# Performance work log

Measured on AMD Instinct MI355X. Metric: run time of the kernel, lower is better.

Reference implementation:

```python
import jax, jax.numpy as jnp
import numpy as np

NUM_HEADS = 16
ROPE_BASE = 10000.0


def apply_rope(x):
    # x: [B, T, H, D]; torchtune-style interleaved-pair RoPE, positions 0..T-1
    B, T, H, D = x.shape
    inv_freq = 1.0 / (ROPE_BASE ** (jnp.arange(0, D, 2, dtype=jnp.float32) / D))  # [D/2]
    pos = jnp.arange(T, dtype=jnp.float32)
    freqs = pos[:, None] * inv_freq[None, :]              # [T, D/2]
    cos = jnp.cos(freqs)[None, :, None, :].astype(x.dtype)
    sin = jnp.sin(freqs)[None, :, None, :].astype(x.dtype)
    x1 = x[..., 0::2]
    x2 = x[..., 1::2]
    o1 = x1 * cos - x2 * sin
    o2 = x2 * cos + x1 * sin
    return jnp.stack([o1, o2], axis=-1).reshape(B, T, H, D)


def setup_inputs() -> dict:
    key = jax.random.key(0)
    k1, k2, k3 = jax.random.split(key, 3)
    B, T, C = 2, 8192, 1024
    x = jax.random.normal(k1, (B, T, C), dtype=jnp.float32)
    # torch Linear weight layout [out_features, in_features]; fan-in scaling
    Wqkv = jax.random.normal(k2, (3 * C, C), dtype=jnp.float32) * (C ** -0.5)
    Wout = jax.random.normal(k3, (C, C), dtype=jnp.float32) * (C ** -0.5)
    return {"x": x, "Wqkv": Wqkv, "Wout": Wout}


def reference(x, Wqkv, Wout):
    B, T, C = x.shape
    H = NUM_HEADS
    D = C // H
    qkv = (x @ Wqkv.T).reshape(B, T, 3, H, D)
    q, k, v = qkv[:, :, 0], qkv[:, :, 1], qkv[:, :, 2]   # each [B, T, H, D]
    q = apply_rope(q)
    k = apply_rope(k)
    # Faithful to source: SDPA is called on [B, T, H, D] WITHOUT transposing,
    # so torch attends over the heads axis (L = H) with (B, T) as batch dims.
    scale = 1.0 / jnp.sqrt(jnp.asarray(D, dtype=x.dtype))
    scores = jnp.einsum('btqd,btkd->btqk', q, k) * scale  # [B, T, H, H]
    attn = jax.nn.softmax(scores, axis=-1)
    out = jnp.einsum('btqk,btkd->btqd', attn, v)          # [B, T, H, D]
    # Replicate attn_output.transpose(1, 2).contiguous().view(B, T, C)
    out = out.transpose(0, 2, 1, 3).reshape(B, T, C)
    return out @ Wout.T
```

## Files before the change

### kernel.cpp

```cpp
#include <hip/hip_runtime.h>
#include <stdint.h>

#define TT 8192
#define BT 16384
#define MCH 8192

typedef __attribute__((ext_vector_type(8))) __bf16 bf16x8;
typedef __attribute__((ext_vector_type(4))) __bf16 bf16x4;
typedef __attribute__((ext_vector_type(4))) short short4v;
typedef __attribute__((ext_vector_type(4))) float floatx4;

__device__ __forceinline__ float bf2f(unsigned short h) {
  union { unsigned u; float f; } x; x.u = ((unsigned)h) << 16; return x.f;
}
__device__ __forceinline__ unsigned short f2bf(float f) {
  union { float f; unsigned u; } x; x.f = f;
  unsigned r = (x.u + 0x7fffu + ((x.u >> 16) & 1u)) >> 16;
  return (unsigned short)r;
}
__device__ __forceinline__ void async16(const void* g, void* l) {
  __builtin_amdgcn_global_load_lds(
      (__attribute__((address_space(1))) void*)g,
      (__attribute__((address_space(3))) void*)l, 16, 0, 0);
}

__global__ __launch_bounds__(256) void cvt_f2b(
    const float* __restrict__ src, unsigned short* __restrict__ dst, int n4) {
  const int i = blockIdx.x * 256 + threadIdx.x;
  if (i < n4) {
    const float4 f = ((const float4*)src)[i];
    union { uint2 u2; unsigned short s[4]; } o;
    o.s[0] = f2bf(f.x); o.s[1] = f2bf(f.y);
    o.s[2] = f2bf(f.z); o.s[3] = f2bf(f.w);
    ((uint2*)dst)[i] = o.u2;
  }
}

__global__ __launch_bounds__(256) void rope_table_k(float2* __restrict__ tab) {
  const int i = blockIdx.x * 256 + threadIdx.x;
  if (i < TT * 32) {
    const int t = i >> 5, p = i & 31;
    const float f = (float)t * exp2f((float)p * -0.41524101186092f);
    float s, c;
    sincosf(f, &s, &c);
    tab[i] = make_float2(c, s);
  }
}

template <bool CF32>
__global__ __launch_bounds__(256) void gemm_bt(
    const unsigned short* __restrict__ A,
    const unsigned short* __restrict__ W,
    void* __restrict__ C,
    int M, int N, int K)
{
  __shared__ __align__(16) unsigned short As[128 * 32];
  __shared__ __align__(16) unsigned short Bs[128 * 32];

  const int tid  = threadIdx.x;
  const int lane = tid & 63;
  const int w    = tid >> 6;
  const int nb   = N / 128;
  const int bm   = blockIdx.x / nb;
  const int bn   = blockIdx.x % nb;
  const int wm   = w & 1;
  const int wn   = w >> 1;
  const int kg   = lane >> 4;
  const int lm   = lane & 15;
  const int srow = lane >> 2;
  const int sch  = lane & 3;

  floatx4 acc[4][4];
  floatx4 z = {0.f, 0.f, 0.f, 0.f};
#pragma unroll
  for (int i = 0; i < 4; ++i)
#pragma unroll
    for (int j = 0; j < 4; ++j) acc[i][j] = z;

  const size_t abase = (size_t)(bm * 128) * K;
  const size_t bbase = (size_t)(bn * 128) * K;

  for (int kt = 0; kt < K; kt += 32) {
#pragma unroll
    for (int s2 = 0; s2 < 2; ++s2) {
      const int s   = 2 * w + s2;
      const int row = 16 * s + srow;
      async16(A + abase + (size_t)row * K + kt + sch * 8, (char*)As + s * 1024);
      async16(W + bbase + (size_t)row * K + kt + sch * 8, (char*)Bs + s * 1024);
    }
    __syncthreads();

    bf16x8 af[4], bfr[4];
#pragma unroll
    for (int i = 0; i < 4; ++i) {
      const int r = wm * 64 + i * 16 + lm;
      af[i] = *(const bf16x8*)(As + r * 32 + kg * 8);
    }
#pragma unroll
    for (int j = 0; j < 4; ++j) {
      const int r = wn * 64 + j * 16 + lm;
      bfr[j] = *(const bf16x8*)(Bs + r * 32 + kg * 8);
    }
#pragma unroll
    for (int i = 0; i < 4; ++i)
#pragma unroll
      for (int j = 0; j < 4; ++j)
        acc[i][j] = __builtin_amdgcn_mfma_f32_16x16x32_bf16(af[i], bfr[j], acc[i][j], 0, 0, 0);
    __syncthreads();
  }

#pragma unroll
  for (int i = 0; i < 4; ++i) {
    const int row0 = bm * 128 + wm * 64 + i * 16 + kg * 4;
#pragma unroll
    for (int j = 0; j < 4; ++j) {
      const int col = bn * 128 + wn * 64 + j * 16 + lm;
#pragma unroll
      for (int r = 0; r < 4; ++r) {
        if (CF32)
          ((float*)C)[(size_t)(row0 + r) * N + col] = acc[i][j][r];
        else
          ((unsigned short*)C)[(size_t)(row0 + r) * N + col] = f2bf(acc[i][j][r]);
      }
    }
  }
}

#if defined(__has_builtin)
#if __has_builtin(__builtin_amdgcn_mfma_f32_16x16x16_bf16)
#define PV_MFMA 1
#define PV_MFMA_CALL(a, b, c) __builtin_amdgcn_mfma_f32_16x16x16_bf16( \
    *(bf16x4*)&(a), *(bf16x4*)&(b), (c), 0, 0, 0)
#elif __has_builtin(__builtin_amdgcn_mfma_f32_16x16x16bf16_1k)
#define PV_MFMA 1
#define PV_MFMA_CALL(a, b, c) __builtin_amdgcn_mfma_f32_16x16x16bf16_1k( \
    (a), (b), (c), 0, 0, 0)
#else
#define PV_MFMA 0
#endif
#else
#define PV_MFMA 0
#endif

__global__ __launch_bounds__(128) void attn_rope_k(
    const unsigned short* __restrict__ qkv,
    const float2* __restrict__ tab,
    unsigned short* __restrict__ Y,
    int base)
{
  __shared__ __align__(16) unsigned short sQKV[2][3 * 16 * 72];
#if !PV_MFMA
  __shared__ float sP[2][256];
#endif

  const int wave = threadIdx.x >> 6;
  const int lane = threadIdx.x & 63;
  const int ml = blockIdx.x * 2 + wave;
  const int m  = base + ml;
  const int t  = m & (TT - 1);
  const int b  = m >> 13;

  unsigned short* QB = sQKV[wave];
  unsigned short* KB = QB + 16 * 72;
  unsigned short* VB = QB + 2 * 16 * 72;

  const int lm   = lane & 15;
  const int quad = lane >> 4;

  const uint4* row = (const uint4*)(qkv + (size_t)ml * 3072);
#pragma unroll
  for (int i = 0; i < 6; ++i) {
    const int c = lane + 64 * i;
    union { uint4 u4; unsigned short s[8]; } cv;
    cv.u4 = row[c];
    const int n0   = c * 8;
    const int part = n0 >> 10;
    const int h    = (n0 >> 6) & 15;
    const int d0   = n0 & 63;
    if (part < 2) {
      float f[8];
#pragma unroll
      for (int j = 0; j < 8; ++j) f[j] = bf2f(cv.s[j]);
      const int p0 = d0 >> 1;
      const float4 csA = *(const float4*)(tab + (t << 5) + p0);
      const float4 csB = *(const float4*)(tab + (t << 5) + p0 + 2);
      const float cs[4] = {csA.x, csA.z, csB.x, csB.z};
      const float sn[4] = {csA.y, csA.w, csB.y, csB.w};
#pragma unroll
      for (int j = 0; j < 4; ++j) {
        const float x1 = f[2 * j], x2 = f[2 * j + 1];
        cv.s[2 * j]     = f2bf(x1 * cs[j] - x2 * sn[j]);
        cv.s[2 * j + 1] = f2bf(x2 * cs[j] + x1 * sn[j]);
      }
    }
    unsigned short* dst = QB + part * (16 * 72) + h * 72 + d0;
    *(uint4*)dst = cv.u4;
  }
  __syncthreads();

  floatx4 accS = {0.f, 0.f, 0.f, 0.f};
#pragma unroll
  for (int half = 0; half < 2; ++half) {
    const bf16x8 kf = *(const bf16x8*)(KB + lm * 72 + half * 32 + quad * 8);
    const bf16x8 qf = *(const bf16x8*)(QB + lm * 72 + half * 32 + quad * 8);
    accS = __builtin_amdgcn_mfma_f32_16x16x32_bf16(kf, qf, accS, 0, 0, 0);
  }
  float s4[4];
  float mx = -1e30f;
#pragma unroll
  for (int j = 0; j < 4; ++j) { s4[j] = accS[j] * 0.125f; mx = fmaxf(mx, s4[j]); }
  mx = fmaxf(mx, __shfl_xor(mx, 16, 64));
  mx = fmaxf(mx, __shfl_xor(mx, 32, 64));
  float sum = 0.f;
#pragma unroll
  for (int j = 0; j < 4; ++j) { s4[j] = __expf(s4[j] - mx); sum += s4[j]; }
  sum += __shfl_xor(sum, 16, 64);
  sum += __shfl_xor(sum, 32, 64);
  const float inv = 1.0f / sum;

#if PV_MFMA
  union { short4v v; unsigned short s[4]; } pf;
#pragma unroll
  for (int j = 0; j < 4; ++j) pf.s[j] = s4[j] * inv == 0.f ? 0 : f2bf(s4[j] * inv);
#pragma unroll
  for (int dtile = 0; dtile < 4; ++dtile) {
    union { short4v v; unsigned short s[4]; } vf;
#pragma unroll
    for (int j = 0; j < 4; ++j)
      vf.s[j] = VB[(quad * 4 + j) * 72 + dtile * 16 + lm];
    floatx4 accO = {0.f, 0.f, 0.f, 0.f};
    accO = PV_MFMA_CALL(pf.v, vf.v, accO);
    const int col = (t & 15) * 64 + dtile * 16 + lm;
#pragma unroll
    for (int r = 0; r < 4; ++r) {
      const size_t rr = (size_t)b * TT + (size_t)(quad * 4 + r) * 512 + (t >> 4);
      Y[rr * 1024 + col] = f2bf(accO[r]);
    }
  }
#else
  float* P = sP[wave];
#pragma unroll
  for (int j = 0; j < 4; ++j) P[(quad * 4 + j) * 16 + lm] = s4[j] * inv;
  __syncthreads();
  float o[16];
#pragma unroll
  for (int dd = 0; dd < 16; ++dd) o[dd] = 0.f;
#pragma unroll
  for (int kh = 0; kh < 16; ++kh) {
    const float a = P[kh * 16 + lm];
    union { uint4 u4; unsigned short s[8]; } v0, v1;
    v0.u4 = *(const uint4*)(VB + kh * 72 + quad * 16);
    v1.u4 = *(const uint4*)(VB + kh * 72 + quad * 16 + 8);
#pragma unroll
    for (int dd = 0; dd < 8; ++dd) {
      o[dd]     += a * bf2f(v0.s[dd]);
      o[dd + 8] += a * bf2f(v1.s[dd]);
    }
  }
  const size_t rr = (size_t)b * TT + (size_t)lm * 512 + (t >> 4);
  unsigned short* yp = Y + rr * 1024 + (t & 15) * 64 + quad * 16;
  union { uint4 u4; unsigned short s[8]; } o1, o2;
#pragma unroll
  for (int dd = 0; dd < 8; ++dd) o1.s[dd] = f2bf(o[dd]);
#pragma unroll
  for (int dd = 0; dd < 8; ++dd) o2.s[dd] = f2bf(o[8 + dd]);
  ((uint4*)yp)[0] = o1.u4;
  ((uint4*)yp)[1] = o2.u4;
#endif
}

extern "C" void kernel_launch(void* const* d_in, const int* in_sizes, int n_in,
                              void* d_out, int out_size, void* d_ws, size_t ws_size,
                              hipStream_t stream) {
  const float* x    = (const float*)d_in[0];
  const float* Wqkv = (const float*)d_in[1];
  const float* Wout = (const float*)d_in[2];
  float* out = (float*)d_out;

  unsigned short* Y     = (unsigned short*)d_ws;
  unsigned short* Wqkvb = Y + (size_t)BT * 1024;
  unsigned short* Woutb = Wqkvb + (size_t)3072 * 1024;
  unsigned short* xb    = Woutb + (size_t)1024 * 1024;
  unsigned short* qkvC  = (unsigned short*)d_out;
  float2* tab           = (float2*)((char*)d_out + (size_t)52 * 1024 * 1024);

  rope_table_k<<<dim3(TT * 32 / 256), dim3(256), 0, stream>>>(tab);
  cvt_f2b<<<dim3(3072 * 1024 / 4 / 256), dim3(256), 0, stream>>>(Wqkv, Wqkvb, 3072 * 1024 / 4);
  cvt_f2b<<<dim3(1024 * 1024 / 4 / 256), dim3(256), 0, stream>>>(Wout, Woutb, 1024 * 1024 / 4);

  for (int base = 0; base < BT; base += MCH) {
    cvt_f2b<<<dim3(MCH * 1024 / 4 / 256), dim3(256), 0, stream>>>(
        x + (size_t)base * 1024, xb, MCH * 1024 / 4);
    gemm_bt<false><<<dim3((MCH / 128) * (3072 / 128)), dim3(256), 0, stream>>>(
        xb, Wqkvb, qkvC, MCH, 3072, 1024);
    attn_rope_k<<<dim3(MCH / 2), dim3(128), 0, stream>>>(qkvC, tab, Y, base);
  }

  gemm_bt<true><<<dim3((BT / 128) * (1024 / 128)), dim3(256), 0, stream>>>(
      Y, Woutb, out, BT, 1024, 1024);
}
```

Baseline: 357.3 us.

## Replace GEMM with 256x256-tile double-buffered pipelined kernel with swizzled LDS

Replaces the 128x128, single-buffered, K=32 GEMM with a 256x256 tile kernel using 8 waves and a K-step of 64. It double-buffers LDS with staggered async global-to-LDS loads, XOR-swizzles LDS columns to avoid bank conflicts, and remaps block IDs for cache locality. It also raises MFMA priority and uses fine-grained waitcnt and barriers so loads overlap compute. The aim is to raise MFMA utilisation and cut the load-then-sync stalls of the old kernel, at the cost of more LDS and registers per block and fewer, larger blocks.

```diff
diff --git a/kernel.cpp b/kernel.cpp
--- a/kernel.cpp
+++ b/kernel.cpp
@@ -48,73 +48,136 @@
 }
 
 template <bool CF32>
-__global__ __launch_bounds__(256) void gemm_bt(
+__global__ __launch_bounds__(512, 2) void gemm256(
     const unsigned short* __restrict__ A,
     const unsigned short* __restrict__ W,
     void* __restrict__ C,
     int M, int N, int K)
 {
-  __shared__ __align__(16) unsigned short As[128 * 32];
-  __shared__ __align__(16) unsigned short Bs[128 * 32];
+  __shared__ __align__(16) unsigned short sm[2][2][256 * 64];
 
   const int tid  = threadIdx.x;
   const int lane = tid & 63;
-  const int w    = tid >> 6;
-  const int nb   = N / 128;
-  const int bm   = blockIdx.x / nb;
-  const int bn   = blockIdx.x % nb;
-  const int wm   = w & 1;
-  const int wn   = w >> 1;
+  const int wid  = tid >> 6;
+  const int wr   = wid >> 2;
+  const int wc   = wid & 3;
+  const int lm   = lane & 15;
   const int kg   = lane >> 4;
-  const int lm   = lane & 15;
-  const int srow = lane >> 2;
-  const int sch  = lane & 3;
-
-  floatx4 acc[4][4];
+
+  const int nb  = N >> 8;
+  const int cpx = (int)gridDim.x >> 3;
+  const int bid = blockIdx.x;
+  const int swz = (bid & 7) * cpx + (bid >> 3);
+  const int bm  = swz / nb;
+  const int bn  = swz % nb;
+
+  const int NT = K >> 6;
+
+  const int srow = lane >> 3;
+  const int sc   = (lane & 7) ^ srow;
+
+  auto stage = [&](const unsigned short* __restrict__ G, size_t grow0,
+                   int kcol, unsigned short* lds) {
+#pragma unroll
+    for (int q = 0; q < 2; ++q) {
+      const int seg = q * 8 + wid;
+      const int r   = seg * 8 + srow;
+      async16(G + (grow0 + (size_t)r) * (size_t)K + kcol + sc * 8,
+              (char*)lds + seg * 1024);
+    }
+  };
+
+  floatx4 acc[8][4];
   floatx4 z = {0.f, 0.f, 0.f, 0.f};
 #pragma unroll
-  for (int i = 0; i < 4; ++i)
+  for (int i = 0; i < 8; ++i)
 #pragma unroll
     for (int j = 0; j < 4; ++j) acc[i][j] = z;
 
-  const size_t abase = (size_t)(bm * 128) * K;
-  const size_t bbase = (size_t)(bn * 128) * K;
-
-  for (int kt = 0; kt < K; kt += 32) {
-#pragma unroll
-    for (int s2 = 0; s2 < 2; ++s2) {
-      const int s   = 2 * w + s2;
-      const int row = 16 * s + srow;
-      async16(A + abase + (size_t)row * K + kt + sch * 8, (char*)As + s * 1024);
-      async16(W + bbase + (size_t)row * K + kt + sch * 8, (char*)Bs + s * 1024);
-    }
-    __syncthreads();
-
-    bf16x8 af[4], bfr[4];
-#pragma unroll
-    for (int i = 0; i < 4; ++i) {
-      const int r = wm * 64 + i * 16 + lm;
-      af[i] = *(const bf16x8*)(As + r * 32 + kg * 8);
-    }
+  const size_t arow = (size_t)bm * 256;
+  const size_t brow = (size_t)bn * 256;
+
+  stage(A, arow,       0, &sm[0][0][0]);
+  stage(A, arow + 128, 0, &sm[0][0][128 * 64]);
+  stage(W, brow,       0, &sm[0][1][0]);
+  stage(W, brow + 128, 0, &sm[0][1][128 * 64]);
+  if (NT > 1) {
+    stage(W, brow,       64, &sm[1][1][0]);
+    stage(W, brow + 128, 64, &sm[1][1][128 * 64]);
+  }
+  asm volatile("s_waitcnt vmcnt(4)" ::: "memory");
+  __builtin_amdgcn_s_barrier();
+  __builtin_amdgcn_sched_barrier(0);
+
+  const int cxor = lm & 7;
+
+  for (int t = 0; t < NT; ++t) {
+    const int buf = t & 1;
+    const unsigned short* Ab = &sm[buf][0][0];
+    const unsigned short* Bb = &sm[buf][1][0];
+    bf16x8 bfrag[4][2];
+
+#pragma unroll
+    for (int p = 0; p < 4; ++p) {
+      bf16x8 afrag[2][2];
+#pragma unroll
+      for (int ii = 0; ii < 2; ++ii) {
+        const int rr = wr * 128 + (p * 2 + ii) * 16 + lm;
+#pragma unroll
+        for (int kk = 0; kk < 2; ++kk)
+          afrag[ii][kk] =
+              *(const bf16x8*)(Ab + rr * 64 + (((kk << 2) + kg) ^ cxor) * 8);
+      }
+      if (p == 0) {
+#pragma unroll
+        for (int j = 0; j < 4; ++j) {
+          const int rr = wc * 64 + j * 16 + lm;
+#pragma unroll
+          for (int kk = 0; kk < 2; ++kk)
+            bfrag[j][kk] =
+                *(const bf16x8*)(Bb + rr * 64 + (((kk << 2) + kg) ^ cxor) * 8);
+        }
+      }
+
+      if (p < 2) {
+        if (t + 1 < NT)
+          stage(A, arow + p * 128, (t + 1) * 64,
+                &sm[buf ^ 1][0][p * 128 * 64]);
+      } else {
+        if (t + 2 < NT)
+          stage(W, brow + (p - 2) * 128, (t + 2) * 64,
+                &sm[buf][1][(p - 2) * 128 * 64]);
+      }
+
+      __builtin_amdgcn_s_barrier();
+      asm volatile("s_waitcnt lgkmcnt(0)" ::: "memory");
+      __builtin_amdgcn_sched_barrier(0);
+
+      __builtin_amdgcn_s_setprio(1);
+#pragma unroll
+      for (int ii = 0; ii < 2; ++ii)
+#pragma unroll
+        for (int j = 0; j < 4; ++j)
+#pragma unroll
+          for (int kk = 0; kk < 2; ++kk)
+            acc[p * 2 + ii][j] = __builtin_amdgcn_mfma_f32_16x16x32_bf16(
+                afrag[ii][kk], bfrag[j][kk], acc[p * 2 + ii][j], 0, 0, 0);
+      __builtin_amdgcn_s_setprio(0);
+
+      if (p == 3) {
+        asm volatile("s_waitcnt vmcnt(4)" ::: "memory");
+      }
+      __builtin_amdgcn_s_barrier();
+      if (p == 3) __builtin_amdgcn_sched_barrier(0);
+    }
+  }
+
+#pragma unroll
+  for (int i = 0; i < 8; ++i) {
+    const int row0 = bm * 256 + wr * 128 + i * 16 + kg * 4;
 #pragma unroll
     for (int j = 0; j < 4; ++j) {
-      const int r = wn * 64 + j * 16 + lm;
-      bfr[j] = *(const bf16x8*)(Bs + r * 32 + kg * 8);
-    }
-#pragma unroll
-    for (int i = 0; i < 4; ++i)
-#pragma unroll
-      for (int j = 0; j < 4; ++j)
-        acc[i][j] = __builtin_amdgcn_mfma_f32_16x16x32_bf16(af[i], bfr[j], acc[i][j], 0, 0, 0);
-    __syncthreads();
-  }
-
-#pragma unroll
-  for (int i = 0; i < 4; ++i) {
-    const int row0 = bm * 128 + wm * 64 + i * 16 + kg * 4;
-#pragma unroll
-    for (int j = 0; j < 4; ++j) {
-      const int col = bn * 128 + wn * 64 + j * 16 + lm;
+      const int col = bn * 256 + wc * 64 + j * 16 + lm;
 #pragma unroll
       for (int r = 0; r < 4; ++r) {
         if (CF32)
@@ -291,11 +354,11 @@
   for (int base = 0; base < BT; base += MCH) {
     cvt_f2b<<<dim3(MCH * 1024 / 4 / 256), dim3(256), 0, stream>>>(
         x + (size_t)base * 1024, xb, MCH * 1024 / 4);
-    gemm_bt<false><<<dim3((MCH / 128) * (3072 / 128)), dim3(256), 0, stream>>>(
+    gemm256<false><<<dim3((MCH / 256) * (3072 / 256)), dim3(512), 0, stream>>>(
         xb, Wqkvb, qkvC, MCH, 3072, 1024);
     attn_rope_k<<<dim3(MCH / 2), dim3(128), 0, stream>>>(qkvC, tab, Y, base);
   }
 
-  gemm_bt<true><<<dim3((BT / 128) * (1024 / 128)), dim3(256), 0, stream>>>(
+  gemm256<true><<<dim3((BT / 256) * (1024 / 256)), dim3(512), 0, stream>>>(
       Y, Woutb, out, BT, 1024, 1024);
 }
```

Measured after the change: 321.9 us. -9.9%, faster.

## Double-buffer GEMM LDS tiles with 256x128 blocks, XOR swizzle, block remap

Applied to the files above, without the earlier changes.

Replaces the single-buffered 128x128 GEMM with a 512-thread, 256x128-tile kernel. The kernel double-buffers LDS and prefetches two K-tiles ahead with async global-to-LDS loads, using explicit waitcnt and barriers instead of two full syncthreads per iteration. It also XOR-swizzles LDS columns to cut bank conflicts, remaps block IDs across 8 groups for cache locality, and raises wave priority around the MFMA block. The goal is to hide global load latency behind compute, at the cost of more LDS per block and hand-managed synchronisation that is fragile to get right.

```diff
diff --git a/kernel.cpp b/kernel.cpp
--- a/kernel.cpp
+++ b/kernel.cpp
@@ -48,27 +48,56 @@
 }
 
 template <bool CF32>
-__global__ __launch_bounds__(256) void gemm_bt(
+__global__ __launch_bounds__(512, 4) void gemm_k32(
     const unsigned short* __restrict__ A,
     const unsigned short* __restrict__ W,
     void* __restrict__ C,
     int M, int N, int K)
 {
-  __shared__ __align__(16) unsigned short As[128 * 32];
-  __shared__ __align__(16) unsigned short Bs[128 * 32];
+  __shared__ __align__(16) unsigned short sm[2][(256 + 128) * 32];
 
   const int tid  = threadIdx.x;
   const int lane = tid & 63;
-  const int w    = tid >> 6;
-  const int nb   = N / 128;
-  const int bm   = blockIdx.x / nb;
-  const int bn   = blockIdx.x % nb;
-  const int wm   = w & 1;
-  const int wn   = w >> 1;
+  const int wid  = tid >> 6;
+  const int wr   = wid >> 1;
+  const int wc   = wid & 1;
+  const int lm   = lane & 15;
   const int kg   = lane >> 4;
-  const int lm   = lane & 15;
-  const int srow = lane >> 2;
-  const int sch  = lane & 3;
+  const int cxor = (lm >> 1) & 3;
+
+  const int nb  = N >> 7;
+  const int cpx = (int)gridDim.x >> 3;
+  const int bid = blockIdx.x;
+  const int swz = (bid & 7) * cpx + (bid >> 3);
+  const int bm  = swz / nb;
+  const int bn  = swz % nb;
+
+  const int NT = K >> 5;
+
+  const int sr  = lane >> 2;
+  const int scb = lane & 3;
+  const unsigned short* gsrc0;
+  const unsigned short* gsrc1;
+  const unsigned short* gsrc2;
+  {
+    const int r0 = wid * 16 + sr;
+    const int r1 = 128 + r0;
+    const int rB = wid * 16 + sr;
+    gsrc0 = A + (size_t)(bm * 256 + r0) * (size_t)K + ((scb ^ ((r0 >> 1) & 3)) << 3);
+    gsrc1 = A + (size_t)(bm * 256 + r1) * (size_t)K + ((scb ^ ((r1 >> 1) & 3)) << 3);
+    gsrc2 = W + (size_t)(bn * 128 + rB) * (size_t)K + ((scb ^ ((rB >> 1) & 3)) << 3);
+  }
+  const int ld0 = wid * 1024;
+  const int ld1 = 8192 + wid * 1024;
+  const int ld2 = 16384 + wid * 1024;
+
+  auto stage_tile = [&](int tt) {
+    char* lb = (char*)sm[tt & 1];
+    const size_t koff = (size_t)tt << 5;
+    async16(gsrc0 + koff, lb + ld0);
+    async16(gsrc1 + koff, lb + ld1);
+    async16(gsrc2 + koff, lb + ld2);
+  };
 
   floatx4 acc[4][4];
   floatx4 z = {0.f, 0.f, 0.f, 0.f};
@@ -77,44 +106,59 @@
 #pragma unroll
     for (int j = 0; j < 4; ++j) acc[i][j] = z;
 
-  const size_t abase = (size_t)(bm * 128) * K;
-  const size_t bbase = (size_t)(bn * 128) * K;
-
-  for (int kt = 0; kt < K; kt += 32) {
-#pragma unroll
-    for (int s2 = 0; s2 < 2; ++s2) {
-      const int s   = 2 * w + s2;
-      const int row = 16 * s + srow;
-      async16(A + abase + (size_t)row * K + kt + sch * 8, (char*)As + s * 1024);
-      async16(W + bbase + (size_t)row * K + kt + sch * 8, (char*)Bs + s * 1024);
-    }
-    __syncthreads();
+  stage_tile(0);
+  stage_tile(1);
+  asm volatile("s_waitcnt vmcnt(3)" ::: "memory");
+  __builtin_amdgcn_s_barrier();
+  __builtin_amdgcn_sched_barrier(0);
+
+  for (int t = 0; t < NT; ++t) {
+    const unsigned short* Ab = sm[t & 1];
+    const unsigned short* Bb = Ab + 256 * 32;
 
     bf16x8 af[4], bfr[4];
 #pragma unroll
     for (int i = 0; i < 4; ++i) {
-      const int r = wm * 64 + i * 16 + lm;
-      af[i] = *(const bf16x8*)(As + r * 32 + kg * 8);
+      const int rr = wr * 64 + i * 16 + lm;
+      af[i] = *(const bf16x8*)(Ab + rr * 32 + ((kg ^ cxor) << 3));
     }
 #pragma unroll
     for (int j = 0; j < 4; ++j) {
-      const int r = wn * 64 + j * 16 + lm;
-      bfr[j] = *(const bf16x8*)(Bs + r * 32 + kg * 8);
-    }
+      const int rr = wc * 64 + j * 16 + lm;
+      bfr[j] = *(const bf16x8*)(Bb + rr * 32 + ((kg ^ cxor) << 3));
+    }
+
+    __builtin_amdgcn_s_barrier();
+    asm volatile("s_waitcnt lgkmcnt(0)" ::: "memory");
+    __builtin_amdgcn_sched_barrier(0);
+
+    if (t + 2 < NT) stage_tile(t + 2);
+
+    __builtin_amdgcn_s_setprio(1);
 #pragma unroll
     for (int i = 0; i < 4; ++i)
 #pragma unroll
       for (int j = 0; j < 4; ++j)
-        acc[i][j] = __builtin_amdgcn_mfma_f32_16x16x32_bf16(af[i], bfr[j], acc[i][j], 0, 0, 0);
-    __syncthreads();
+        acc[i][j] = __builtin_amdgcn_mfma_f32_16x16x32_bf16(
+            af[i], bfr[j], acc[i][j], 0, 0, 0);
+    __builtin_amdgcn_s_setprio(0);
+
+    if (t + 1 < NT) {
+      if (t + 2 < NT)
+        asm volatile("s_waitcnt vmcnt(3)" ::: "memory");
+      else
+        asm volatile("s_waitcnt vmcnt(0)" ::: "memory");
+      __builtin_amdgcn_s_barrier();
+      __builtin_amdgcn_sched_barrier(0);
+    }
   }
 
 #pragma unroll
   for (int i = 0; i < 4; ++i) {
-    const int row0 = bm * 128 + wm * 64 + i * 16 + kg * 4;
+    const int row0 = bm * 256 + wr * 64 + i * 16 + kg * 4;
 #pragma unroll
     for (int j = 0; j < 4; ++j) {
-      const int col = bn * 128 + wn * 64 + j * 16 + lm;
+      const int col = bn * 128 + wc * 64 + j * 16 + lm;
 #pragma unroll
       for (int r = 0; r < 4; ++r) {
         if (CF32)
@@ -291,11 +335,11 @@
   for (int base = 0; base < BT; base += MCH) {
     cvt_f2b<<<dim3(MCH * 1024 / 4 / 256), dim3(256), 0, stream>>>(
         x + (size_t)base * 1024, xb, MCH * 1024 / 4);
-    gemm_bt<false><<<dim3((MCH / 128) * (3072 / 128)), dim3(256), 0, stream>>>(
+    gemm_k32<false><<<dim3((MCH / 256) * (3072 / 128)), dim3(512), 0, stream>>>(
         xb, Wqkvb, qkvC, MCH, 3072, 1024);
     attn_rope_k<<<dim3(MCH / 2), dim3(128), 0, stream>>>(qkvC, tab, Y, base);
   }
 
-  gemm_bt<true><<<dim3((BT / 128) * (1024 / 128)), dim3(256), 0, stream>>>(
+  gemm_k32<true><<<dim3((BT / 256) * (1024 / 128)), dim3(512), 0, stream>>>(
       Y, Woutb, out, BT, 1024, 1024);
 }
```

Result: faster. 311.7 us (-12.8%).

## Rewrite GEMMs with pre-packed weight fragments, triple-buffered swizzled A tiles, larger blocks

Applied to the files above, without the earlier changes.

Weights are now packed once into an MFMA-fragment-ordered bf16 layout, so each wave loads its B fragments directly from global memory into registers, double-buffered, and no longer stages them through LDS. A tiles of 256 rows are staged asynchronously into a three-deep LDS ring with an XOR swizzle to avoid bank conflicts. Explicit vmcnt waits and a single barrier per k-step give a software pipeline. Blocks grow to 512 threads with 256x192 or 256x128 tiles, a grid swizzle improves L2 locality, and setprio is raised around the MFMA bursts. This cuts LDS traffic and barrier stalls, at the cost of higher register pressure and fragile hand-tuned waitcnt counts.

```diff
diff --git a/kernel.cpp b/kernel.cpp
--- a/kernel.cpp
+++ b/kernel.cpp
@@ -36,6 +36,25 @@
   }
 }
 
+__global__ __launch_bounds__(256) void pack_w(
+    const float* __restrict__ src, uint4* __restrict__ dst, int nchunks,
+    int K, int NT) {
+  const int c = blockIdx.x * 256 + threadIdx.x;
+  if (c >= nchunks) return;
+  const int l  = c & 63;
+  const int g  = c >> 6;
+  const int kt = g % NT;
+  const int rb = g / NT;
+  const int row = rb * 16 + (l & 15);
+  const int k0  = kt * 32 + (l >> 4) * 8;
+  const float4 f0 = *(const float4*)(src + (size_t)row * K + k0);
+  const float4 f1 = *(const float4*)(src + (size_t)row * K + k0 + 4);
+  union { uint4 u4; unsigned short s[8]; } o;
+  o.s[0] = f2bf(f0.x); o.s[1] = f2bf(f0.y); o.s[2] = f2bf(f0.z); o.s[3] = f2bf(f0.w);
+  o.s[4] = f2bf(f1.x); o.s[5] = f2bf(f1.y); o.s[6] = f2bf(f1.z); o.s[7] = f2bf(f1.w);
+  dst[c] = o.u4;
+}
+
 __global__ __launch_bounds__(256) void rope_table_k(float2* __restrict__ tab) {
   const int i = blockIdx.x * 256 + threadIdx.x;
   if (i < TT * 32) {
@@ -47,74 +66,132 @@
   }
 }
 
-template <bool CF32>
-__global__ __launch_bounds__(256) void gemm_bt(
+template <int NWF, bool CF32>
+__global__ __launch_bounds__(512, 2) void gemm_bd(
     const unsigned short* __restrict__ A,
-    const unsigned short* __restrict__ W,
+    const uint4* __restrict__ Wp,
     void* __restrict__ C,
     int M, int N, int K)
 {
-  __shared__ __align__(16) unsigned short As[128 * 32];
-  __shared__ __align__(16) unsigned short Bs[128 * 32];
-
+  __shared__ __align__(16) unsigned short smA[3 * 256 * 32];
+
+  const int BN   = 2 * NWF * 16;
   const int tid  = threadIdx.x;
   const int lane = tid & 63;
-  const int w    = tid >> 6;
-  const int nb   = N / 128;
-  const int bm   = blockIdx.x / nb;
-  const int bn   = blockIdx.x % nb;
-  const int wm   = w & 1;
-  const int wn   = w >> 1;
+  const int wid  = tid >> 6;
+  const int wr   = wid >> 1;
+  const int wcl  = wid & 1;
+  const int lm   = lane & 15;
   const int kg   = lane >> 4;
-  const int lm   = lane & 15;
-  const int srow = lane >> 2;
-  const int sch  = lane & 3;
-
-  floatx4 acc[4][4];
+  const int cxor = (lm >> 1) & 3;
+
+  const int nbm = M >> 8;
+  const int cpx = (int)gridDim.x >> 3;
+  const int bid = blockIdx.x;
+  const int swz = (bid & 7) * cpx + (bid >> 3);
+  const int bm  = swz % nbm;
+  const int bn  = swz / nbm;
+
+  const int NT = K >> 5;
+
+  const unsigned short* gsrcA0;
+  const unsigned short* gsrcA1;
+  int ldso0, ldso1;
+  {
+    const int i0 = tid, i1 = 512 + tid;
+    const int r0 = i0 >> 2, c0 = i0 & 3;
+    const int r1 = i1 >> 2, c1 = i1 & 3;
+    gsrcA0 = A + (size_t)(bm * 256 + r0) * (size_t)K + ((c0 ^ ((r0 >> 1) & 3)) << 3);
+    gsrcA1 = A + (size_t)(bm * 256 + r1) * (size_t)K + ((c1 ^ ((r1 >> 1) & 3)) << 3);
+    ldso0 = i0 * 8;
+    ldso1 = i1 * 8;
+  }
+#define STAGE_A(tt)                                                      \
+  {                                                                      \
+    unsigned short* d = smA + ((tt) % 3) * 8192;                         \
+    async16(gsrcA0 + (size_t)(tt) * 32, d + ldso0);                      \
+    async16(gsrcA1 + (size_t)(tt) * 32, d + ldso1);                      \
+  }
+
+  const int rbg0 = bn * (BN >> 4) + wcl * NWF;
+  const uint4* WpJ[NWF];
+#pragma unroll
+  for (int j = 0; j < NWF; ++j)
+    WpJ[j] = Wp + ((size_t)(rbg0 + j) * (size_t)NT) * 64 + lane;
+
+  floatx4 acc[4][NWF];
   floatx4 z = {0.f, 0.f, 0.f, 0.f};
 #pragma unroll
   for (int i = 0; i < 4; ++i)
 #pragma unroll
-    for (int j = 0; j < 4; ++j) acc[i][j] = z;
-
-  const size_t abase = (size_t)(bm * 128) * K;
-  const size_t bbase = (size_t)(bn * 128) * K;
-
-  for (int kt = 0; kt < K; kt += 32) {
-#pragma unroll
-    for (int s2 = 0; s2 < 2; ++s2) {
-      const int s   = 2 * w + s2;
-      const int row = 16 * s + srow;
-      async16(A + abase + (size_t)row * K + kt + sch * 8, (char*)As + s * 1024);
-      async16(W + bbase + (size_t)row * K + kt + sch * 8, (char*)Bs + s * 1024);
-    }
-    __syncthreads();
-
-    bf16x8 af[4], bfr[4];
-#pragma unroll
-    for (int i = 0; i < 4; ++i) {
-      const int r = wm * 64 + i * 16 + lm;
-      af[i] = *(const bf16x8*)(As + r * 32 + kg * 8);
-    }
-#pragma unroll
-    for (int j = 0; j < 4; ++j) {
-      const int r = wn * 64 + j * 16 + lm;
-      bfr[j] = *(const bf16x8*)(Bs + r * 32 + kg * 8);
-    }
-#pragma unroll
-    for (int i = 0; i < 4; ++i)
-#pragma unroll
-      for (int j = 0; j < 4; ++j)
-        acc[i][j] = __builtin_amdgcn_mfma_f32_16x16x32_bf16(af[i], bfr[j], acc[i][j], 0, 0, 0);
-    __syncthreads();
-  }
+    for (int j = 0; j < NWF; ++j) acc[i][j] = z;
+
+  bf16x8 Bbuf0[NWF], Bbuf1[NWF];
+
+#pragma unroll
+  for (int j = 0; j < NWF; ++j)
+    Bbuf0[j] = *(const bf16x8*)(WpJ[j]);
+  STAGE_A(0);
+  STAGE_A(1);
+  asm volatile("s_waitcnt vmcnt(2)" ::: "memory");
+  __builtin_amdgcn_sched_barrier(0);
+
+#define SUBITER(T, BC, BNX)                                                   \
+  {                                                                           \
+    const int t_ = (T);                                                       \
+    __builtin_amdgcn_s_barrier();                                             \
+    const unsigned short* Ab = smA + (t_ % 3) * 8192;                         \
+    bf16x8 afr[4];                                                            \
+    _Pragma("unroll")                                                         \
+    for (int i = 0; i < 4; ++i) {                                             \
+      const int rr = wr * 64 + i * 16 + lm;                                   \
+      afr[i] = *(const bf16x8*)(Ab + rr * 32 + ((kg ^ cxor) << 3));           \
+    }                                                                         \
+    if (t_ + 1 < NT) {                                                        \
+      _Pragma("unroll")                                                       \
+      for (int j = 0; j < NWF; ++j)                                           \
+        BNX[j] = *(const bf16x8*)(WpJ[j] + (size_t)(t_ + 1) * 64);            \
+    }                                                                         \
+    if (t_ + 2 < NT) STAGE_A(t_ + 2);                                         \
+    if (t_ + 2 < NT) {                                                        \
+      if constexpr (NWF == 6)                                                 \
+        asm volatile("s_waitcnt vmcnt(8)" ::: "memory");                      \
+      else                                                                    \
+        asm volatile("s_waitcnt vmcnt(6)" ::: "memory");                      \
+    } else if (t_ + 1 < NT) {                                                 \
+      if constexpr (NWF == 6)                                                 \
+        asm volatile("s_waitcnt vmcnt(6)" ::: "memory");                      \
+      else                                                                    \
+        asm volatile("s_waitcnt vmcnt(4)" ::: "memory");                      \
+    } else {                                                                  \
+      asm volatile("s_waitcnt vmcnt(0)" ::: "memory");                        \
+    }                                                                         \
+    asm volatile("s_waitcnt lgkmcnt(0)" ::: "memory");                        \
+    __builtin_amdgcn_sched_barrier(0);                                        \
+    __builtin_amdgcn_s_setprio(1);                                            \
+    _Pragma("unroll")                                                         \
+    for (int i = 0; i < 4; ++i)                                               \
+      _Pragma("unroll")                                                       \
+      for (int j = 0; j < NWF; ++j)                                           \
+        acc[i][j] = __builtin_amdgcn_mfma_f32_16x16x32_bf16(                  \
+            afr[i], BC[j], acc[i][j], 0, 0, 0);                               \
+    __builtin_amdgcn_s_setprio(0);                                            \
+    __builtin_amdgcn_sched_barrier(0);                                        \
+  }
+
+  for (int t = 0; t < NT; t += 2) {
+    SUBITER(t, Bbuf0, Bbuf1);
+    SUBITER(t + 1, Bbuf1, Bbuf0);
+  }
+#undef SUBITER
+#undef STAGE_A
 
 #pragma unroll
   for (int i = 0; i < 4; ++i) {
-    const int row0 = bm * 128 + wm * 64 + i * 16 + kg * 4;
-#pragma unroll
-    for (int j = 0; j < 4; ++j) {
-      const int col = bn * 128 + wn * 64 + j * 16 + lm;
+    const int row0 = bm * 256 + wr * 64 + i * 16 + kg * 4;
+#pragma unroll
+    for (int j = 0; j < NWF; ++j) {
+      const int col = bn * BN + wcl * (NWF * 16) + j * 16 + lm;
 #pragma unroll
       for (int r = 0; r < 4; ++r) {
         if (CF32)
@@ -278,24 +355,26 @@
   float* out = (float*)d_out;
 
   unsigned short* Y     = (unsigned short*)d_ws;
-  unsigned short* Wqkvb = Y + (size_t)BT * 1024;
-  unsigned short* Woutb = Wqkvb + (size_t)3072 * 1024;
-  unsigned short* xb    = Woutb + (size_t)1024 * 1024;
+  unsigned short* Wqkvp = Y + (size_t)BT * 1024;
+  unsigned short* Woutp = Wqkvp + (size_t)3072 * 1024;
+  unsigned short* xb    = Woutp + (size_t)1024 * 1024;
   unsigned short* qkvC  = (unsigned short*)d_out;
   float2* tab           = (float2*)((char*)d_out + (size_t)52 * 1024 * 1024);
 
   rope_table_k<<<dim3(TT * 32 / 256), dim3(256), 0, stream>>>(tab);
-  cvt_f2b<<<dim3(3072 * 1024 / 4 / 256), dim3(256), 0, stream>>>(Wqkv, Wqkvb, 3072 * 1024 / 4);
-  cvt_f2b<<<dim3(1024 * 1024 / 4 / 256), dim3(256), 0, stream>>>(Wout, Woutb, 1024 * 1024 / 4);
+  pack_w<<<dim3(3072 * 1024 / 8 / 256), dim3(256), 0, stream>>>(
+      Wqkv, (uint4*)Wqkvp, 3072 * 1024 / 8, 1024, 32);
+  pack_w<<<dim3(1024 * 1024 / 8 / 256), dim3(256), 0, stream>>>(
+      Wout, (uint4*)Woutp, 1024 * 1024 / 8, 1024, 32);
 
   for (int base = 0; base < BT; base += MCH) {
     cvt_f2b<<<dim3(MCH * 1024 / 4 / 256), dim3(256), 0, stream>>>(
         x + (size_t)base * 1024, xb, MCH * 1024 / 4);
-    gemm_bt<false><<<dim3((MCH / 128) * (3072 / 128)), dim3(256), 0, stream>>>(
-        xb, Wqkvb, qkvC, MCH, 3072, 1024);
+    gemm_bd<6, false><<<dim3((MCH / 256) * (3072 / 192)), dim3(512), 0, stream>>>(
+        xb, (const uint4*)Wqkvp, qkvC, MCH, 3072, 1024);
     attn_rope_k<<<dim3(MCH / 2), dim3(128), 0, stream>>>(qkvC, tab, Y, base);
   }
 
-  gemm_bt<true><<<dim3((BT / 128) * (1024 / 128)), dim3(256), 0, stream>>>(
-      Y, Woutb, out, BT, 1024, 1024);
-}
+  gemm_bd<4, true><<<dim3((BT / 256) * (1024 / 128)), dim3(512), 0, stream>>>(
+      Y, (const uint4*)Woutp, out, BT, 1024, 1024);
+}
```

Result: slower. 365.9 us (+2.4%).
